# Kernel optimization log

Measured on AMD Instinct MI355X. Metric: run time of the kernel, lower is better.

The kernel has to match this reference:

```python
import jax, jax.numpy as jnp
import numpy as np

N_POINTS = 64
N_DIM = 2 * N_POINTS          # 128
N_CONTROL = 2
FC = [1024, 1024]
DT = 0.1
ELEMS_A = 4 * N_POINTS        # 256 (computed but unused, matching original)
ELEMS_B = N_DIM * N_CONTROL   # 256


def setup_inputs() -> dict:
    key = jax.random.key(0)
    ks = jax.random.split(key, 8)
    B, T = 4096, 64
    states = jax.random.normal(ks[0], (B, T, N_DIM), dtype=jnp.float32)
    actions = jax.random.normal(ks[1], (B, T, N_CONTROL), dtype=jnp.float32)
    d_in = N_DIM + N_CONTROL  # 130
    scale = lambda fan_in: 1.0 / np.sqrt(fan_in)
    W1 = jax.random.normal(ks[2], (d_in, FC[0]), dtype=jnp.float32) * scale(d_in)
    b1 = jnp.zeros((FC[0],), dtype=jnp.float32)
    W2 = jax.random.normal(ks[3], (FC[0], FC[1]), dtype=jnp.float32) * scale(FC[0])
    b2 = jnp.zeros((FC[1],), dtype=jnp.float32)
    W3 = jax.random.normal(ks[4], (FC[1], ELEMS_A + ELEMS_B), dtype=jnp.float32) * scale(FC[1])
    b3 = jnp.zeros((ELEMS_A + ELEMS_B,), dtype=jnp.float32)
    return {"states": states, "actions": actions,
            "W1": W1, "b1": b1, "W2": W2, "b2": b2, "W3": W3, "b3": b3}


def reference(states, actions, W1, b1, W2, b2, W3, b3):
    # states: [B, T, n_dim], actions: [B, T, 2]
    s0 = states[:, 0]  # [B, n_dim]
    actions_t = jnp.swapaxes(actions, 0, 1)  # [T, B, 2]

    def step(s, a):
        z = jnp.concatenate([s, a], axis=1)          # [B, n_dim+2]
        z = jax.nn.relu(z @ W1 + b1)
        z = jax.nn.relu(z @ W2 + b2)
        params = z @ W3 + b3                          # [B, elems_A + elems_B]
        # A_t params (params[:, :ELEMS_A]) are computed but unused in the original update.
        B_params = params[:, ELEMS_A:]                # [B, 4*n_points]
        Bmat = B_params.reshape(-1, N_DIM, N_CONTROL) # block rows: [B, 2*n_points, 2]
        s_next = s + jnp.einsum('bnc,bc->bn', Bmat, a) * DT
        return s_next, s_next

    _, traj = jax.lax.scan(step, s0, actions_t)       # traj: [T, B, n_dim]
    gen = jnp.concatenate([s0[:, None], jnp.swapaxes(traj, 0, 1)], axis=1)
    return gen  # [B, T+1, n_dim]
```

## Files before the change

### kernel.cpp

```cpp
#include <hip/hip_runtime.h>
#include <stdint.h>

#define B_SZ 4096
#define T_SZ 64
#define ND   128
#define HID  1024
#define PO   256

typedef __attribute__((ext_vector_type(8))) short bf16x8;
typedef __attribute__((ext_vector_type(4))) float f32x4;

__device__ __forceinline__ unsigned short f2bf(float x) {
  unsigned int u = __float_as_uint(x);
  u += 0x7fffu + ((u >> 16) & 1u);
  return (unsigned short)(u >> 16);
}
__device__ __forceinline__ float bf2f(unsigned short h) {
  return __uint_as_float(((unsigned int)h) << 16);
}

__device__ __forceinline__ void g2lds(const void* g, void* l) {
  __builtin_amdgcn_global_load_lds(
      (const __attribute__((address_space(1))) unsigned int*)g,
      (__attribute__((address_space(3))) unsigned int*)l, 16, 0, 0);
}

template <int BM, int BN, int MT, int NT, int EPI>
__global__ __launch_bounds__(256, 1) void gemm_split(
    const unsigned short* __restrict__ Ahi, const unsigned short* __restrict__ Alo,
    const unsigned short* __restrict__ Bhi, const unsigned short* __restrict__ Blo,
    const float* __restrict__ bias, int K, int ldc,
    const float* __restrict__ a_t, const float* __restrict__ w1r,
    unsigned short* __restrict__ Zhi, unsigned short* __restrict__ Zlo,
    float* __restrict__ Pout) {
  constexpr int BK = 32;
  static_assert(BM == BN, "square tiles only");
  constexpr int RA = (BM * BK * 2) / 4096;
  __shared__ __attribute__((aligned(16))) unsigned short AsH[BM * BK];
  __shared__ __attribute__((aligned(16))) unsigned short AsL[BM * BK];
  __shared__ __attribute__((aligned(16))) unsigned short BsH[BN * BK];
  __shared__ __attribute__((aligned(16))) unsigned short BsL[BN * BK];

  const int tid  = threadIdx.x;
  const int lane = tid & 63;
  const int wave = tid >> 6;
  const int wm = (wave >> 1) * (MT * 16);
  const int wn = (wave & 1) * (NT * 16);
  const int m0 = blockIdx.x * BM;
  const int n0 = blockIdx.y * BN;
  const size_t Kb = (size_t)K * 2;

  size_t gA[RA], gB[RA];
  int lL[RA];
#pragma unroll
  for (int r = 0; r < RA; ++r) {
    int L = (r * 256 + tid) * 16;
    int row = L >> 6;
    int colb = L & 63;
    lL[r] = L;
    gA[r] = (size_t)(m0 + row) * Kb + colb;
    gB[r] = (size_t)(n0 + row) * Kb + colb;
  }

  f32x4 acc[MT][NT] = {};
  const char* Ah = (const char*)Ahi;
  const char* Al = (const char*)Alo;
  const char* Bh = (const char*)Bhi;
  const char* Bl = (const char*)Blo;
  char* asH = (char*)AsH; char* asL = (char*)AsL;
  char* bsH = (char*)BsH; char* bsL = (char*)BsL;

  const int kIt = K / BK;
  for (int it = 0; it < kIt; ++it) {
    const size_t kadd = (size_t)it * (BK * 2);
#pragma unroll
    for (int r = 0; r < RA; ++r) {
      g2lds(Ah + gA[r] + kadd, asH + lL[r]);
      g2lds(Al + gA[r] + kadd, asL + lL[r]);
      g2lds(Bh + gB[r] + kadd, bsH + lL[r]);
      g2lds(Bl + gB[r] + kadd, bsL + lL[r]);
    }
    __syncthreads();

    bf16x8 fa_h[MT], fa_l[MT], fb_h[NT], fb_l[NT];
#pragma unroll
    for (int mt = 0; mt < MT; ++mt) {
      int off = (wm + mt * 16 + (lane & 15)) * BK + (lane >> 4) * 8;
      fa_h[mt] = *(const bf16x8*)&AsH[off];
      fa_l[mt] = *(const bf16x8*)&AsL[off];
    }
#pragma unroll
    for (int nt = 0; nt < NT; ++nt) {
      int off = (wn + nt * 16 + (lane & 15)) * BK + (lane >> 4) * 8;
      fb_h[nt] = *(const bf16x8*)&BsH[off];
      fb_l[nt] = *(const bf16x8*)&BsL[off];
    }
#pragma unroll
    for (int mt = 0; mt < MT; ++mt)
#pragma unroll
      for (int nt = 0; nt < NT; ++nt) {
        acc[mt][nt] = __builtin_amdgcn_mfma_f32_16x16x32_bf16(fa_h[mt], fb_h[nt], acc[mt][nt], 0, 0, 0);
        acc[mt][nt] = __builtin_amdgcn_mfma_f32_16x16x32_bf16(fa_l[mt], fb_h[nt], acc[mt][nt], 0, 0, 0);
        acc[mt][nt] = __builtin_amdgcn_mfma_f32_16x16x32_bf16(fa_h[mt], fb_l[nt], acc[mt][nt], 0, 0, 0);
      }
    __syncthreads();
  }

#pragma unroll
  for (int mt = 0; mt < MT; ++mt) {
    const int mb = m0 + wm + mt * 16 + ((lane >> 4) << 2);
    float a0v[4], a1v[4];
    if (EPI == 1) {
#pragma unroll
      for (int r = 0; r < 4; ++r) {
        a0v[r] = a_t[(mb + r) * 2];
        a1v[r] = a_t[(mb + r) * 2 + 1];
      }
    }
#pragma unroll
    for (int nt = 0; nt < NT; ++nt) {
      const int n = n0 + wn + nt * 16 + (lane & 15);
      const float bv = bias[n];
      float w0 = 0.f, w1 = 0.f;
      if (EPI == 1) { w0 = w1r[n]; w1 = w1r[HID + n]; }
#pragma unroll
      for (int r = 0; r < 4; ++r) {
        float v = acc[mt][nt][r] + bv;
        if (EPI == 1) v += a0v[r] * w0 + a1v[r] * w1;
        const size_t idx = (size_t)(mb + r) * ldc + n;
        if (EPI == 0) {
          Pout[idx] = v;
        } else {
          v = fmaxf(v, 0.f);
          unsigned short h = f2bf(v);
          Zhi[idx] = h;
          Zlo[idx] = f2bf(v - bf2f(h));
        }
      }
    }
  }
}

__global__ void prep_kernel(
    const float* __restrict__ states, const float* __restrict__ actions,
    const float* __restrict__ W1, const float* __restrict__ W2,
    const float* __restrict__ W3,
    unsigned short* __restrict__ W1tH, unsigned short* __restrict__ W1tL,
    unsigned short* __restrict__ W2tH, unsigned short* __restrict__ W2tL,
    unsigned short* __restrict__ W3tH, unsigned short* __restrict__ W3tL,
    float* __restrict__ aT, float* __restrict__ s,
    unsigned short* __restrict__ sH, unsigned short* __restrict__ sL,
    float* __restrict__ gen) {
  const int tid = blockIdx.x * blockDim.x + threadIdx.x;
  const int stride = gridDim.x * blockDim.x;
  for (int i = tid; i < ND * HID; i += stride) {
    int k = i >> 10, j = i & 1023;
    float v = W1[i];
    unsigned short h = f2bf(v);
    W1tH[j * ND + k] = h;
    W1tL[j * ND + k] = f2bf(v - bf2f(h));
  }
  for (int i = tid; i < HID * HID; i += stride) {
    int k = i >> 10, j = i & 1023;
    float v = W2[i];
    unsigned short h = f2bf(v);
    W2tH[j * HID + k] = h;
    W2tL[j * HID + k] = f2bf(v - bf2f(h));
  }
  for (int i = tid; i < HID * PO; i += stride) {
    int k = i >> 8, j = i & 255;
    float v = W3[k * 512 + 256 + j];
    unsigned short h = f2bf(v);
    W3tH[j * HID + k] = h;
    W3tL[j * HID + k] = f2bf(v - bf2f(h));
  }
  for (int i = tid; i < B_SZ * T_SZ; i += stride) {
    int b = i >> 6, t = i & 63;
    float2 v = ((const float2*)actions)[i];
    ((float2*)aT)[t * B_SZ + b] = v;
  }
  for (int i = tid; i < B_SZ * ND; i += stride) {
    int b = i >> 7, n = i & 127;
    float v = states[(size_t)b * (T_SZ * ND) + n];
    s[i] = v;
    unsigned short h = f2bf(v);
    sH[i] = h;
    sL[i] = f2bf(v - bf2f(h));
    gen[(size_t)b * ((T_SZ + 1) * ND) + n] = v;
  }
}

__global__ void update_kernel(const float* __restrict__ P, const float* __restrict__ a_t,
                              float* __restrict__ s, unsigned short* __restrict__ sH,
                              unsigned short* __restrict__ sL, float* __restrict__ gen,
                              int t) {
  int i = blockIdx.x * 256 + threadIdx.x;
  int b = i >> 7, n = i & 127;
  float2 p = ((const float2*)P)[(size_t)b * 128 + n];
  float a0 = a_t[b * 2], a1 = a_t[b * 2 + 1];
  float v = s[i] + (p.x * a0 + p.y * a1) * 0.1f;
  s[i] = v;
  unsigned short h = f2bf(v);
  sH[i] = h;
  sL[i] = f2bf(v - bf2f(h));
  gen[(size_t)b * ((T_SZ + 1) * ND) + (size_t)(t + 1) * ND + n] = v;
}

extern "C" void kernel_launch(void* const* d_in, const int* in_sizes, int n_in,
                              void* d_out, int out_size, void* d_ws, size_t ws_size,
                              hipStream_t stream) {
  const float* states  = (const float*)d_in[0];
  const float* actions = (const float*)d_in[1];
  const float* W1 = (const float*)d_in[2];
  const float* b1 = (const float*)d_in[3];
  const float* W2 = (const float*)d_in[4];
  const float* b2 = (const float*)d_in[5];
  const float* W3 = (const float*)d_in[6];
  const float* b3 = (const float*)d_in[7];
  float* gen = (float*)d_out;

  char* w = (char*)d_ws;
  float*          s    = (float*)(w + 0);
  unsigned short* sH   = (unsigned short*)(w + (2ull << 20));
  unsigned short* sL   = (unsigned short*)(w + (3ull << 20));
  unsigned short* z1H  = (unsigned short*)(w + (4ull << 20));
  unsigned short* z1L  = (unsigned short*)(w + (12ull << 20));
  unsigned short* z2H  = (unsigned short*)(w + (20ull << 20));
  unsigned short* z2L  = (unsigned short*)(w + (28ull << 20));
  float*          P    = (float*)(w + (36ull << 20));
  float*          aT   = (float*)(w + (40ull << 20));
  unsigned short* W1tH = (unsigned short*)(w + (42ull << 20));
  unsigned short* W1tL = (unsigned short*)(w + (42ull << 20) + 262144);
  unsigned short* W2tH = (unsigned short*)(w + (43ull << 20));
  unsigned short* W2tL = (unsigned short*)(w + (45ull << 20));
  unsigned short* W3tH = (unsigned short*)(w + (47ull << 20));
  unsigned short* W3tL = (unsigned short*)(w + (47ull << 20) + 524288);

  prep_kernel<<<2048, 256, 0, stream>>>(states, actions, W1, W2, W3,
      W1tH, W1tL, W2tH, W2tL, W3tH, W3tL, aT, s, sH, sL, gen);

  const float* w1r = W1 + 128 * 1024;
  for (int t = 0; t < 64; ++t) {
    const float* at = aT + (size_t)t * B_SZ * 2;
    gemm_split<128, 128, 4, 4, 1><<<dim3(32, 8), 256, 0, stream>>>(
        sH, sL, W1tH, W1tL, b1, 128, HID, at, w1r, z1H, z1L, (float*)nullptr);
    gemm_split<128, 128, 4, 4, 2><<<dim3(32, 8), 256, 0, stream>>>(
        z1H, z1L, W2tH, W2tL, b2, HID, HID, (const float*)nullptr,
        (const float*)nullptr, z2H, z2L, (float*)nullptr);
    gemm_split<64, 64, 2, 2, 0><<<dim3(64, 4), 256, 0, stream>>>(
        z2H, z2L, W3tH, W3tL, b3 + 256, HID, PO, (const float*)nullptr,
        (const float*)nullptr, (unsigned short*)nullptr, (unsigned short*)nullptr, P);
    update_kernel<<<2048, 256, 0, stream>>>(P, at, s, sH, sL, gen, t);
  }
}
```

Baseline: 5.495 ms.

## Fuse state update into third GEMM epilogue, retile GEMMs, tiled weight transposes

Folds the per-step state update (B-matrix times action, scaled add, bf16 hi/lo split, writing gen) into the epilogue of the third GEMM. Adjacent output columns are combined with a lane shuffle, so the P buffer round-trip and one launch per step go away. The first two GEMMs switch to 512 threads, BK=64 and 8 waves in a 4x2 layout, which halves the K-loop barriers and changes occupancy. The one-time prep is replaced by LDS-tiled transpose kernels that give coalesced weight and action transposes. The fused epilogue puts half the lanes idle during the state writes, and the wider tiles double LDS per block.

```diff
diff --git a/kernel.cpp b/kernel.cpp
--- a/kernel.cpp
+++ b/kernel.cpp
@@ -25,17 +25,18 @@
       (__attribute__((address_space(3))) unsigned int*)l, 16, 0, 0);
 }
 
-template <int BM, int BN, int MT, int NT, int EPI>
-__global__ __launch_bounds__(256, 1) void gemm_split(
+template <int BM, int BN, int BK, int MT, int NT, int NWY, int EPI, int T>
+__global__ __launch_bounds__(T) void gemm_split(
     const unsigned short* __restrict__ Ahi, const unsigned short* __restrict__ Alo,
     const unsigned short* __restrict__ Bhi, const unsigned short* __restrict__ Blo,
     const float* __restrict__ bias, int K, int ldc,
     const float* __restrict__ a_t, const float* __restrict__ w1r,
     unsigned short* __restrict__ Zhi, unsigned short* __restrict__ Zlo,
-    float* __restrict__ Pout) {
-  constexpr int BK = 32;
-  static_assert(BM == BN, "square tiles only");
-  constexpr int RA = (BM * BK * 2) / 4096;
+    float* __restrict__ s, unsigned short* __restrict__ sH,
+    unsigned short* __restrict__ sL, float* __restrict__ gen, int tstep) {
+  constexpr int ROWB = BK * 2;
+  constexpr int RA = (BM * ROWB) / (T * 16);
+  static_assert(BM == BN && BM * ROWB == RA * T * 16, "tile/thread mismatch");
   __shared__ __attribute__((aligned(16))) unsigned short AsH[BM * BK];
   __shared__ __attribute__((aligned(16))) unsigned short AsL[BM * BK];
   __shared__ __attribute__((aligned(16))) unsigned short BsH[BN * BK];
@@ -44,8 +45,8 @@
   const int tid  = threadIdx.x;
   const int lane = tid & 63;
   const int wave = tid >> 6;
-  const int wm = (wave >> 1) * (MT * 16);
-  const int wn = (wave & 1) * (NT * 16);
+  const int wm = (wave / NWY) * (MT * 16);
+  const int wn = (wave % NWY) * (NT * 16);
   const int m0 = blockIdx.x * BM;
   const int n0 = blockIdx.y * BN;
   const size_t Kb = (size_t)K * 2;
@@ -54,9 +55,9 @@
   int lL[RA];
 #pragma unroll
   for (int r = 0; r < RA; ++r) {
-    int L = (r * 256 + tid) * 16;
-    int row = L >> 6;
-    int colb = L & 63;
+    int L = (r * T + tid) * 16;
+    int row = L / ROWB;
+    int colb = L % ROWB;
     lL[r] = L;
     gA[r] = (size_t)(m0 + row) * Kb + colb;
     gB[r] = (size_t)(n0 + row) * Kb + colb;
@@ -72,7 +73,7 @@
 
   const int kIt = K / BK;
   for (int it = 0; it < kIt; ++it) {
-    const size_t kadd = (size_t)it * (BK * 2);
+    const size_t kadd = (size_t)it * ROWB;
 #pragma unroll
     for (int r = 0; r < RA; ++r) {
       g2lds(Ah + gA[r] + kadd, asH + lL[r]);
@@ -82,56 +83,68 @@
     }
     __syncthreads();
 
-    bf16x8 fa_h[MT], fa_l[MT], fb_h[NT], fb_l[NT];
-#pragma unroll
-    for (int mt = 0; mt < MT; ++mt) {
-      int off = (wm + mt * 16 + (lane & 15)) * BK + (lane >> 4) * 8;
-      fa_h[mt] = *(const bf16x8*)&AsH[off];
-      fa_l[mt] = *(const bf16x8*)&AsL[off];
+#pragma unroll
+    for (int ks = 0; ks < BK / 32; ++ks) {
+      bf16x8 fa_h[MT], fa_l[MT], fb_h[NT], fb_l[NT];
+#pragma unroll
+      for (int mt = 0; mt < MT; ++mt) {
+        int off = (wm + mt * 16 + (lane & 15)) * BK + ks * 32 + (lane >> 4) * 8;
+        fa_h[mt] = *(const bf16x8*)&AsH[off];
+        fa_l[mt] = *(const bf16x8*)&AsL[off];
+      }
+#pragma unroll
+      for (int nt = 0; nt < NT; ++nt) {
+        int off = (wn + nt * 16 + (lane & 15)) * BK + ks * 32 + (lane >> 4) * 8;
+        fb_h[nt] = *(const bf16x8*)&BsH[off];
+        fb_l[nt] = *(const bf16x8*)&BsL[off];
+      }
+#pragma unroll
+      for (int mt = 0; mt < MT; ++mt)
+#pragma unroll
+        for (int nt = 0; nt < NT; ++nt) {
+          acc[mt][nt] = __builtin_amdgcn_mfma_f32_16x16x32_bf16(fa_h[mt], fb_h[nt], acc[mt][nt], 0, 0, 0);
+          acc[mt][nt] = __builtin_amdgcn_mfma_f32_16x16x32_bf16(fa_l[mt], fb_h[nt], acc[mt][nt], 0, 0, 0);
+          acc[mt][nt] = __builtin_amdgcn_mfma_f32_16x16x32_bf16(fa_h[mt], fb_l[nt], acc[mt][nt], 0, 0, 0);
+        }
     }
-#pragma unroll
-    for (int nt = 0; nt < NT; ++nt) {
-      int off = (wn + nt * 16 + (lane & 15)) * BK + (lane >> 4) * 8;
-      fb_h[nt] = *(const bf16x8*)&BsH[off];
-      fb_l[nt] = *(const bf16x8*)&BsL[off];
-    }
-#pragma unroll
-    for (int mt = 0; mt < MT; ++mt)
-#pragma unroll
-      for (int nt = 0; nt < NT; ++nt) {
-        acc[mt][nt] = __builtin_amdgcn_mfma_f32_16x16x32_bf16(fa_h[mt], fb_h[nt], acc[mt][nt], 0, 0, 0);
-        acc[mt][nt] = __builtin_amdgcn_mfma_f32_16x16x32_bf16(fa_l[mt], fb_h[nt], acc[mt][nt], 0, 0, 0);
-        acc[mt][nt] = __builtin_amdgcn_mfma_f32_16x16x32_bf16(fa_h[mt], fb_l[nt], acc[mt][nt], 0, 0, 0);
-      }
     __syncthreads();
   }
 
 #pragma unroll
   for (int mt = 0; mt < MT; ++mt) {
     const int mb = m0 + wm + mt * 16 + ((lane >> 4) << 2);
-    float a0v[4], a1v[4];
-    if (EPI == 1) {
-#pragma unroll
-      for (int r = 0; r < 4; ++r) {
-        a0v[r] = a_t[(mb + r) * 2];
-        a1v[r] = a_t[(mb + r) * 2 + 1];
-      }
-    }
 #pragma unroll
     for (int nt = 0; nt < NT; ++nt) {
       const int n = n0 + wn + nt * 16 + (lane & 15);
       const float bv = bias[n];
-      float w0 = 0.f, w1 = 0.f;
-      if (EPI == 1) { w0 = w1r[n]; w1 = w1r[HID + n]; }
-#pragma unroll
-      for (int r = 0; r < 4; ++r) {
-        float v = acc[mt][nt][r] + bv;
-        if (EPI == 1) v += a0v[r] * w0 + a1v[r] * w1;
-        const size_t idx = (size_t)(mb + r) * ldc + n;
-        if (EPI == 0) {
-          Pout[idx] = v;
-        } else {
+      if (EPI == 3) {
+        const int ns = n >> 1;
+#pragma unroll
+        for (int r = 0; r < 4; ++r) {
+          const int row = mb + r;
+          float v = acc[mt][nt][r] + bv;
+          float av = a_t[row * 2 + (n & 1)];
+          float w = v * av * 0.1f;
+          float wsum = w + __shfl_xor(w, 1);
+          if (!(lane & 1)) {
+            const int si = row * ND + ns;
+            float sn = s[si] + wsum;
+            s[si] = sn;
+            unsigned short h = f2bf(sn);
+            sH[si] = h;
+            sL[si] = f2bf(sn - bf2f(h));
+            gen[(size_t)row * ((T_SZ + 1) * ND) + (size_t)(tstep + 1) * ND + ns] = sn;
+          }
+        }
+      } else {
+        float w0 = 0.f, w1 = 0.f;
+        if (EPI == 1) { w0 = w1r[n]; w1 = w1r[HID + n]; }
+#pragma unroll
+        for (int r = 0; r < 4; ++r) {
+          float v = acc[mt][nt][r] + bv;
+          if (EPI == 1) v += a_t[(mb + r) * 2] * w0 + a_t[(mb + r) * 2 + 1] * w1;
           v = fmaxf(v, 0.f);
+          const size_t idx = (size_t)(mb + r) * ldc + n;
           unsigned short h = f2bf(v);
           Zhi[idx] = h;
           Zlo[idx] = f2bf(v - bf2f(h));
@@ -141,69 +154,53 @@
   }
 }
 
-__global__ void prep_kernel(
-    const float* __restrict__ states, const float* __restrict__ actions,
-    const float* __restrict__ W1, const float* __restrict__ W2,
-    const float* __restrict__ W3,
-    unsigned short* __restrict__ W1tH, unsigned short* __restrict__ W1tL,
-    unsigned short* __restrict__ W2tH, unsigned short* __restrict__ W2tL,
-    unsigned short* __restrict__ W3tH, unsigned short* __restrict__ W3tL,
-    float* __restrict__ aT, float* __restrict__ s,
+__global__ __launch_bounds__(256) void transpose_split(
+    const float* __restrict__ src, int CS, int R, int colOff,
+    unsigned short* __restrict__ dH, unsigned short* __restrict__ dL) {
+  __shared__ float tile[32][33];
+  const int tx = threadIdx.x & 31, ty = threadIdx.x >> 5;
+  const int r0 = blockIdx.x * 32;
+#pragma unroll
+  for (int j = 0; j < 4; ++j)
+    tile[ty + j * 8][tx] =
+        src[(size_t)(r0 + ty + j * 8) * CS + blockIdx.y * 32 + colOff + tx];
+  __syncthreads();
+#pragma unroll
+  for (int j = 0; j < 4; ++j) {
+    const int c = blockIdx.y * 32 + ty + j * 8;
+    const float v = tile[tx][ty + j * 8];
+    unsigned short h = f2bf(v);
+    dH[(size_t)c * R + r0 + tx] = h;
+    dL[(size_t)c * R + r0 + tx] = f2bf(v - bf2f(h));
+  }
+}
+
+__global__ __launch_bounds__(256) void act_transpose(
+    const float2* __restrict__ acts, float2* __restrict__ aT) {
+  __shared__ float2 tile[32][33];
+  const int tx = threadIdx.x & 31, ty = threadIdx.x >> 5;
+  const int b0 = blockIdx.x * 32, t0 = blockIdx.y * 32;
+#pragma unroll
+  for (int j = 0; j < 4; ++j)
+    tile[ty + j * 8][tx] = acts[(size_t)(b0 + ty + j * 8) * T_SZ + t0 + tx];
+  __syncthreads();
+#pragma unroll
+  for (int j = 0; j < 4; ++j)
+    aT[(size_t)(t0 + ty + j * 8) * B_SZ + b0 + tx] = tile[tx][ty + j * 8];
+}
+
+__global__ __launch_bounds__(256) void init_state(
+    const float* __restrict__ states, float* __restrict__ s,
     unsigned short* __restrict__ sH, unsigned short* __restrict__ sL,
     float* __restrict__ gen) {
-  const int tid = blockIdx.x * blockDim.x + threadIdx.x;
-  const int stride = gridDim.x * blockDim.x;
-  for (int i = tid; i < ND * HID; i += stride) {
-    int k = i >> 10, j = i & 1023;
-    float v = W1[i];
-    unsigned short h = f2bf(v);
-    W1tH[j * ND + k] = h;
-    W1tL[j * ND + k] = f2bf(v - bf2f(h));
-  }
-  for (int i = tid; i < HID * HID; i += stride) {
-    int k = i >> 10, j = i & 1023;
-    float v = W2[i];
-    unsigned short h = f2bf(v);
-    W2tH[j * HID + k] = h;
-    W2tL[j * HID + k] = f2bf(v - bf2f(h));
-  }
-  for (int i = tid; i < HID * PO; i += stride) {
-    int k = i >> 8, j = i & 255;
-    float v = W3[k * 512 + 256 + j];
-    unsigned short h = f2bf(v);
-    W3tH[j * HID + k] = h;
-    W3tL[j * HID + k] = f2bf(v - bf2f(h));
-  }
-  for (int i = tid; i < B_SZ * T_SZ; i += stride) {
-    int b = i >> 6, t = i & 63;
-    float2 v = ((const float2*)actions)[i];
-    ((float2*)aT)[t * B_SZ + b] = v;
-  }
-  for (int i = tid; i < B_SZ * ND; i += stride) {
-    int b = i >> 7, n = i & 127;
-    float v = states[(size_t)b * (T_SZ * ND) + n];
-    s[i] = v;
-    unsigned short h = f2bf(v);
-    sH[i] = h;
-    sL[i] = f2bf(v - bf2f(h));
-    gen[(size_t)b * ((T_SZ + 1) * ND) + n] = v;
-  }
-}
-
-__global__ void update_kernel(const float* __restrict__ P, const float* __restrict__ a_t,
-                              float* __restrict__ s, unsigned short* __restrict__ sH,
-                              unsigned short* __restrict__ sL, float* __restrict__ gen,
-                              int t) {
-  int i = blockIdx.x * 256 + threadIdx.x;
-  int b = i >> 7, n = i & 127;
-  float2 p = ((const float2*)P)[(size_t)b * 128 + n];
-  float a0 = a_t[b * 2], a1 = a_t[b * 2 + 1];
-  float v = s[i] + (p.x * a0 + p.y * a1) * 0.1f;
+  const int i = blockIdx.x * 256 + threadIdx.x;
+  const int b = i >> 7, n = i & 127;
+  const float v = states[(size_t)b * (T_SZ * ND) + n];
   s[i] = v;
   unsigned short h = f2bf(v);
   sH[i] = h;
   sL[i] = f2bf(v - bf2f(h));
-  gen[(size_t)b * ((T_SZ + 1) * ND) + (size_t)(t + 1) * ND + n] = v;
+  gen[(size_t)b * ((T_SZ + 1) * ND) + n] = v;
 }
 
 extern "C" void kernel_launch(void* const* d_in, const int* in_sizes, int n_in,
@@ -227,29 +224,31 @@
   unsigned short* z1L  = (unsigned short*)(w + (12ull << 20));
   unsigned short* z2H  = (unsigned short*)(w + (20ull << 20));
   unsigned short* z2L  = (unsigned short*)(w + (28ull << 20));
-  float*          P    = (float*)(w + (36ull << 20));
-  float*          aT   = (float*)(w + (40ull << 20));
-  unsigned short* W1tH = (unsigned short*)(w + (42ull << 20));
-  unsigned short* W1tL = (unsigned short*)(w + (42ull << 20) + 262144);
-  unsigned short* W2tH = (unsigned short*)(w + (43ull << 20));
-  unsigned short* W2tL = (unsigned short*)(w + (45ull << 20));
-  unsigned short* W3tH = (unsigned short*)(w + (47ull << 20));
-  unsigned short* W3tL = (unsigned short*)(w + (47ull << 20) + 524288);
-
-  prep_kernel<<<2048, 256, 0, stream>>>(states, actions, W1, W2, W3,
-      W1tH, W1tL, W2tH, W2tL, W3tH, W3tL, aT, s, sH, sL, gen);
+  float*          aT   = (float*)(w + (36ull << 20));
+  unsigned short* W1tH = (unsigned short*)(w + (38ull << 20));
+  unsigned short* W1tL = (unsigned short*)(w + (38ull << 20) + 262144);
+  unsigned short* W2tH = (unsigned short*)(w + (39ull << 20));
+  unsigned short* W2tL = (unsigned short*)(w + (41ull << 20));
+  unsigned short* W3tH = (unsigned short*)(w + (43ull << 20));
+  unsigned short* W3tL = (unsigned short*)(w + (43ull << 20) + 524288);
+
+  transpose_split<<<dim3(4, 32), 256, 0, stream>>>(W1, 1024, 128, 0, W1tH, W1tL);
+  transpose_split<<<dim3(32, 32), 256, 0, stream>>>(W2, 1024, 1024, 0, W2tH, W2tL);
+  transpose_split<<<dim3(32, 8), 256, 0, stream>>>(W3, 512, 1024, 256, W3tH, W3tL);
+  act_transpose<<<dim3(128, 2), 256, 0, stream>>>((const float2*)actions, (float2*)aT);
+  init_state<<<2048, 256, 0, stream>>>(states, s, sH, sL, gen);
 
   const float* w1r = W1 + 128 * 1024;
   for (int t = 0; t < 64; ++t) {
     const float* at = aT + (size_t)t * B_SZ * 2;
-    gemm_split<128, 128, 4, 4, 1><<<dim3(32, 8), 256, 0, stream>>>(
-        sH, sL, W1tH, W1tL, b1, 128, HID, at, w1r, z1H, z1L, (float*)nullptr);
-    gemm_split<128, 128, 4, 4, 2><<<dim3(32, 8), 256, 0, stream>>>(
-        z1H, z1L, W2tH, W2tL, b2, HID, HID, (const float*)nullptr,
-        (const float*)nullptr, z2H, z2L, (float*)nullptr);
-    gemm_split<64, 64, 2, 2, 0><<<dim3(64, 4), 256, 0, stream>>>(
-        z2H, z2L, W3tH, W3tL, b3 + 256, HID, PO, (const float*)nullptr,
-        (const float*)nullptr, (unsigned short*)nullptr, (unsigned short*)nullptr, P);
-    update_kernel<<<2048, 256, 0, stream>>>(P, at, s, sH, sL, gen, t);
-  }
-}
+    gemm_split<128, 128, 64, 2, 4, 2, 1, 512><<<dim3(32, 8), 512, 0, stream>>>(
+        sH, sL, W1tH, W1tL, b1, 128, HID, at, w1r, z1H, z1L,
+        nullptr, nullptr, nullptr, nullptr, 0);
+    gemm_split<128, 128, 64, 2, 4, 2, 2, 512><<<dim3(32, 8), 512, 0, stream>>>(
+        z1H, z1L, W2tH, W2tL, b2, HID, HID, nullptr, nullptr, z2H, z2L,
+        nullptr, nullptr, nullptr, nullptr, 0);
+    gemm_split<64, 64, 32, 2, 2, 2, 3, 256><<<dim3(64, 4), 256, 0, stream>>>(
+        z2H, z2L, W3tH, W3tL, b3 + 256, HID, 0, at, nullptr, nullptr, nullptr,
+        s, sH, sL, gen, t);
+  }
+}
```

Result: no change. 5.508 ms (+0.2%).
